# Kernel tuning notes

Hardware: AMD Instinct MI355X
Metric: run time of the kernel (lower is better)

Reference implementation:

```python
import jax, jax.numpy as jnp
import numpy as np

BS, NE, DM, DR = 4, 48, 64, 64

def setup_inputs() -> dict:
    key = jax.random.key(0)
    ks = jax.random.split(key, 8)
    ht = jax.random.normal(ks[0], (BS, NE, NE, DR), dtype=jnp.float32)
    factor = jax.random.normal(ks[1], (BS, NE, NE, NE, DM), dtype=jnp.float32)
    ent_numbers = jax.random.randint(ks[2], (BS,), NE // 2, NE + 1).astype(jnp.int32)
    ent_numbers = ent_numbers.at[0].set(NE)  # max(ent_numbers) must equal ne
    s_c = 1.0 / np.sqrt(DM + DR)
    W_c = jax.random.uniform(ks[3], (DM + DR, DM), jnp.float32, -s_c, s_c)
    b_c = jax.random.uniform(ks[4], (DM,), jnp.float32, -s_c, s_c)
    v_w = jax.random.uniform(ks[5], (DM,), jnp.float32, -1.0 / np.sqrt(DM), 1.0 / np.sqrt(DM))
    s_f = 1.0 / np.sqrt(DM)
    W_fc = jax.random.uniform(ks[6], (DM, DR), jnp.float32, -s_f, s_f)
    b_fc = jax.random.uniform(ks[7], (DR,), jnp.float32, -s_f, s_f)
    ln_g = jnp.ones((DR,), jnp.float32)
    ln_b = jnp.zeros((DR,), jnp.float32)
    return {"ht": ht, "factor": factor, "W_c": W_c, "b_c": b_c, "v_w": v_w,
            "W_fc": W_fc, "b_fc": b_fc, "ln_g": ln_g, "ln_b": ln_b,
            "ent_numbers": ent_numbers}


def reference(ht, factor, W_c, b_c, v_w, W_fc, b_fc, ln_g, ln_b, ent_numbers):
    # factor_type == 'sib'; dropout in eval mode (identity)
    bs, ne, _, dr = ht.shape
    ha = factor                                   # b,i,j,k,dm
    hb = jnp.transpose(factor, (0, 1, 3, 2, 4))   # b,i,k,j,dm -> swap of obj axes
    total_h = jnp.concatenate([ha, hb], axis=3)   # b,i,j,2k,dm
    n2 = total_h.shape[3]
    ht_b = jnp.broadcast_to(ht[:, :, :, None, :], (bs, ne, ne, n2, dr))
    comb = jnp.concatenate([ht_b, total_h], axis=-1)          # b,i,j,2k,dr+dm
    h = jax.nn.gelu(comb @ W_c + b_c, approximate=False)      # exact erf GELU like torch nn.GELU()
    energy = jnp.einsum('bijkd,d->bijk', h, v_w)              # b,i,j,2ne
    # masks: valid[b,e] = e < ent_numbers[b]; mask3d[b,i,j,k] = valid_i & valid_j & valid_k
    idx = jnp.arange(ne)
    valid = idx[None, :] < ent_numbers[:, None]               # b,ne
    mask3d = valid[:, :, None, None] & valid[:, None, :, None] & valid[:, None, None, :]
    eye = jnp.eye(ne, dtype=bool)
    m1 = eye[None, None, :, :] | ~mask3d                      # b,i,j,k  (eye over (j,k))
    attn_mask = jnp.concatenate([m1, m1], axis=-1)            # b,i,j,2ne
    energy = jnp.where(attn_mask, jnp.float32(-10000.0), energy)
    attention = jax.nn.softmax(energy, axis=-1)
    output = jnp.einsum('bijk,bijkd->bijd', attention, total_h)
    output = output @ W_fc + b_fc + ht                        # fc + residual
    mu = jnp.mean(output, axis=-1, keepdims=True)
    var = jnp.mean(jnp.square(output - mu), axis=-1, keepdims=True)
    return ln_g * (output - mu) * jax.lax.rsqrt(var + 1e-6) + ln_b
```

## Files before the change

### kernel.cpp

```cpp
#include <hip/hip_runtime.h>
#include <math.h>
#include <stdint.h>

#define BS 4
#define NE 48
#define DM 64
#define DR 64
#define N2 96

typedef const __attribute__((address_space(1))) uint32_t* gptr_t;
typedef __attribute__((address_space(3))) uint32_t* lptr_t;

__device__ __forceinline__ float wsum(float v) {
#pragma unroll
    for (int m = 1; m < 64; m <<= 1) v += __shfl_xor(v, m, 64);
    return v;
}
__device__ __forceinline__ float wmax(float v) {
#pragma unroll
    for (int m = 1; m < 64; m <<= 1) v = fmaxf(v, __shfl_xor(v, m, 64));
    return v;
}

__device__ __forceinline__ float erf_approx(float x) {
    float ax = fabsf(x);
    float t  = __builtin_amdgcn_rcpf(fmaf(0.3275911f, ax, 1.0f));
    float p  = t * (0.254829592f +
               t * (-0.284496736f +
               t * (1.421413741f +
               t * (-1.453152027f +
               t * 1.061405429f))));
    float e  = __expf(-ax * ax);
    float r  = fmaf(-p, e, 1.0f);
    return copysignf(r, x);
}
__device__ __forceinline__ float gelu_exact(float x) {
    return 0.5f * x * (1.0f + erf_approx(x * 0.70710678118654752440f));
}

__global__ __launch_bounds__(256, 3)
void hgnn_kernel(const float* __restrict__ ht,
                 const float* __restrict__ factor,
                 const float* __restrict__ W_c,
                 const float* __restrict__ b_c,
                 const float* __restrict__ v_w,
                 const float* __restrict__ W_fc,
                 const float* __restrict__ b_fc,
                 const float* __restrict__ ln_g,
                 const float* __restrict__ ln_b,
                 const int* __restrict__ ent_numbers,
                 float* __restrict__ out) {
    __shared__ float sTh[N2][DM];
    __shared__ float sHt[DR];
    __shared__ float sE[N2];
    __shared__ float sA[N2];
    __shared__ float sPart[4][DM];
    __shared__ float sOut[DM];

    const int tid  = threadIdx.x;
    const int lane = tid & 63;
    const int wave = tid >> 6;

    const int orig = blockIdx.x;
    const int bid  = (orig & 7) * (BS * NE * NE / 8) + (orig >> 3);

    const int b   = bid / (NE * NE);
    const int rem = bid - b * NE * NE;
    const int i   = rem / NE;
    const int j   = rem - i * NE;

    const int ent = ent_numbers[b];
    const bool row_valid = (i < ent) && (j < ent);

    {
        const float* fbase = factor + (size_t)((b * NE + i) * NE + j) * NE * DM;
        const float4* srcA = (const float4*)fbase;
#pragma unroll
        for (int n = 0; n < 3; ++n) {
            const int idx0 = n * 256 + wave * 64;
            const float4* g = srcA + idx0 + lane;
            __builtin_amdgcn_global_load_lds(
                (gptr_t)g,
                (lptr_t)((char*)&sTh[0][0] + (size_t)idx0 * 16),
                16, 0, 0);
        }
        const float* fb2 = factor + (size_t)(b * NE + i) * NE * NE * DM + (size_t)j * DM;
#pragma unroll
        for (int n = 0; n < 3; ++n) {
            const int idx0 = n * 256 + wave * 64;
            const int idx  = idx0 + lane;
            const int k    = idx >> 4;
            const int r4   = idx & 15;
            const float4* g = (const float4*)(fb2 + (size_t)k * NE * DM) + r4;
            __builtin_amdgcn_global_load_lds(
                (gptr_t)g,
                (lptr_t)((char*)&sTh[0][0] + (size_t)(NE * 256) + (size_t)idx0 * 16),
                16, 0, 0);
        }
    }

    if (tid < DR) sHt[tid] = ht[((size_t)(b * NE + i) * NE + j) * DR + tid];

    float wcol[64];
#pragma unroll
    for (int r = 0; r < 64; ++r) wcol[r] = W_c[(size_t)(DM + r) * DM + lane];
#pragma unroll
    for (int r = 0; r < 64; ++r) asm volatile("" : "+v"(wcol[r]));

    const float bc = b_c[lane];
    const float vw = v_w[lane];

    __syncthreads();

    float htc = bc;
    {
        const float4* htv = (const float4*)sHt;
#pragma unroll
        for (int r4 = 0; r4 < 16; ++r4) {
            float4 t = htv[r4];
            htc = fmaf(t.x, W_c[(4 * r4 + 0) * DM + lane], htc);
            htc = fmaf(t.y, W_c[(4 * r4 + 1) * DM + lane], htc);
            htc = fmaf(t.z, W_c[(4 * r4 + 2) * DM + lane], htc);
            htc = fmaf(t.w, W_c[(4 * r4 + 3) * DM + lane], htc);
        }
    }

#pragma unroll 1
    for (int t = 0; t < 12; ++t) {
        const int k2a = 8 * t + wave;
        const int k2b = k2a + 4;
        const int ka  = (k2a >= NE) ? (k2a - NE) : k2a;
        const int kb  = (k2b >= NE) ? (k2b - NE) : k2b;
        const bool va = row_valid && (ka != j) && (ka < ent);
        const bool vb = row_valid && (kb != j) && (kb < ent);
        if (!va && !vb) {
            if (lane == 0) { sE[k2a] = -10000.0f; sE[k2b] = -10000.0f; }
            continue;
        }
        float a0 = 0.f, a1 = 0.f, a2 = 0.f, a3 = 0.f;
        float b0 = 0.f, b1 = 0.f, b2 = 0.f, b3 = 0.f;
        const float4* ra = (const float4*)(&sTh[k2a][0]);
        const float4* rb = (const float4*)(&sTh[k2b][0]);
#pragma unroll
        for (int r4 = 0; r4 < 16; ++r4) {
            float4 ta = ra[r4];
            float4 tb = rb[r4];
            a0 = fmaf(ta.x, wcol[4 * r4 + 0], a0);
            b0 = fmaf(tb.x, wcol[4 * r4 + 0], b0);
            a1 = fmaf(ta.y, wcol[4 * r4 + 1], a1);
            b1 = fmaf(tb.y, wcol[4 * r4 + 1], b1);
            a2 = fmaf(ta.z, wcol[4 * r4 + 2], a2);
            b2 = fmaf(tb.z, wcol[4 * r4 + 2], b2);
            a3 = fmaf(ta.w, wcol[4 * r4 + 3], a3);
            b3 = fmaf(tb.w, wcol[4 * r4 + 3], b3);
        }
        float xa = htc + ((a0 + a1) + (a2 + a3));
        float xb = htc + ((b0 + b1) + (b2 + b3));
        float ea = wsum(gelu_exact(xa) * vw);
        float eb = wsum(gelu_exact(xb) * vw);
        if (lane == 0) {
            sE[k2a] = va ? ea : -10000.0f;
            sE[k2b] = vb ? eb : -10000.0f;
        }
    }
    __syncthreads();

    float v0 = sE[lane];
    float v1 = (lane < 32) ? sE[64 + lane] : -3.0e38f;
    float mx = wmax(fmaxf(v0, v1));
    float e0 = expf(v0 - mx);
    float e1 = (lane < 32) ? expf(v1 - mx) : 0.0f;
    float sm = wsum(e0 + e1);
    float inv = 1.0f / sm;
    if (wave == 0) {
        sA[lane] = e0 * inv;
        if (lane < 32) sA[64 + lane] = e1 * inv;
    }
    __syncthreads();

    {
        float acc = 0.0f;
#pragma unroll
        for (int t = 0; t < 24; ++t) {
            const int k2 = 4 * t + wave;
            acc = fmaf(sA[k2], sTh[k2][lane], acc);
        }
        sPart[wave][lane] = acc;
    }
    __syncthreads();
    if (tid < DM)
        sOut[tid] = sPart[0][tid] + sPart[1][tid] + sPart[2][tid] + sPart[3][tid];
    __syncthreads();

    if (wave == 0) {
        float acc = b_fc[lane] + sHt[lane];
        const float4* ov = (const float4*)sOut;
#pragma unroll
        for (int r4 = 0; r4 < 16; ++r4) {
            float4 t4 = ov[r4];
            acc = fmaf(t4.x, W_fc[(4 * r4 + 0) * DM + lane], acc);
            acc = fmaf(t4.y, W_fc[(4 * r4 + 1) * DM + lane], acc);
            acc = fmaf(t4.z, W_fc[(4 * r4 + 2) * DM + lane], acc);
            acc = fmaf(t4.w, W_fc[(4 * r4 + 3) * DM + lane], acc);
        }
        float mu  = wsum(acc) * (1.0f / 64.0f);
        float d   = acc - mu;
        float var = wsum(d * d) * (1.0f / 64.0f);
        float y   = ln_g[lane] * d * rsqrtf(var + 1e-6f) + ln_b[lane];
        out[((size_t)(b * NE + i) * NE + j) * DM + lane] = y;
    }
}

extern "C" void kernel_launch(void* const* d_in, const int* in_sizes, int n_in,
                              void* d_out, int out_size, void* d_ws, size_t ws_size,
                              hipStream_t stream) {
    const float* ht   = (const float*)d_in[0];
    const float* fac  = (const float*)d_in[1];
    const float* W_c  = (const float*)d_in[2];
    const float* b_c  = (const float*)d_in[3];
    const float* v_w  = (const float*)d_in[4];
    const float* W_fc = (const float*)d_in[5];
    const float* b_fc = (const float*)d_in[6];
    const float* ln_g = (const float*)d_in[7];
    const float* ln_b = (const float*)d_in[8];
    const int*   ent  = (const int*)d_in[9];
    float* out = (float*)d_out;

    dim3 grid(BS * NE * NE);
    hgnn_kernel<<<grid, 256, 0, stream>>>(ht, fac, W_c, b_c, v_w, W_fc, b_fc,
                                          ln_g, ln_b, ent, out);
}
```

Baseline: 340.8 us.

## Process four rows per wave iteration, raise occupancy bound, use fast exp in softmax

The energy loop now handles four k-rows per wave per iteration instead of two, with interleaved shuffle reductions for the four sums. Launch bounds go from 3 to 4 blocks per CU and the asm barrier pinning wcol in registers is removed, so the compiler may spill or rematerialize under the tighter budget. The softmax switches expf to __expf. The wider unroll raises ILP and reuses each weight register across more rows, but the stricter register cap risks spills.

```diff
diff --git a/kernel.cpp b/kernel.cpp
--- a/kernel.cpp
+++ b/kernel.cpp
@@ -38,7 +38,7 @@
     return 0.5f * x * (1.0f + erf_approx(x * 0.70710678118654752440f));
 }
 
-__global__ __launch_bounds__(256, 3)
+__global__ __launch_bounds__(256, 4)
 void hgnn_kernel(const float* __restrict__ ht,
                  const float* __restrict__ factor,
                  const float* __restrict__ W_c,
@@ -104,8 +104,6 @@
     float wcol[64];
 #pragma unroll
     for (int r = 0; r < 64; ++r) wcol[r] = W_c[(size_t)(DM + r) * DM + lane];
-#pragma unroll
-    for (int r = 0; r < 64; ++r) asm volatile("" : "+v"(wcol[r]));
 
     const float bc = b_c[lane];
     const float vw = v_w[lane];
@@ -126,41 +124,65 @@
     }
 
 #pragma unroll 1
-    for (int t = 0; t < 12; ++t) {
-        const int k2a = 8 * t + wave;
-        const int k2b = k2a + 4;
-        const int ka  = (k2a >= NE) ? (k2a - NE) : k2a;
-        const int kb  = (k2b >= NE) ? (k2b - NE) : k2b;
-        const bool va = row_valid && (ka != j) && (ka < ent);
-        const bool vb = row_valid && (kb != j) && (kb < ent);
-        if (!va && !vb) {
-            if (lane == 0) { sE[k2a] = -10000.0f; sE[k2b] = -10000.0f; }
+    for (int t = 0; t < 6; ++t) {
+        const int k0 = 16 * t + wave;
+        bool v[4];
+#pragma unroll
+        for (int q = 0; q < 4; ++q) {
+            const int k2 = k0 + 4 * q;
+            const int kk = (k2 >= NE) ? (k2 - NE) : k2;
+            v[q] = row_valid && (kk != j) && (kk < ent);
+        }
+        if (!(v[0] | v[1] | v[2] | v[3])) {
+            if (lane == 0) {
+                sE[k0]      = -10000.0f;
+                sE[k0 + 4]  = -10000.0f;
+                sE[k0 + 8]  = -10000.0f;
+                sE[k0 + 12] = -10000.0f;
+            }
             continue;
         }
-        float a0 = 0.f, a1 = 0.f, a2 = 0.f, a3 = 0.f;
-        float b0 = 0.f, b1 = 0.f, b2 = 0.f, b3 = 0.f;
-        const float4* ra = (const float4*)(&sTh[k2a][0]);
-        const float4* rb = (const float4*)(&sTh[k2b][0]);
+        float ac0 = 0.f, ac1 = 0.f, ac2 = 0.f, ac3 = 0.f;
+        const float4* r0 = (const float4*)(&sTh[k0][0]);
+        const float4* r1 = (const float4*)(&sTh[k0 + 4][0]);
+        const float4* r2 = (const float4*)(&sTh[k0 + 8][0]);
+        const float4* r3 = (const float4*)(&sTh[k0 + 12][0]);
 #pragma unroll
         for (int r4 = 0; r4 < 16; ++r4) {
-            float4 ta = ra[r4];
-            float4 tb = rb[r4];
-            a0 = fmaf(ta.x, wcol[4 * r4 + 0], a0);
-            b0 = fmaf(tb.x, wcol[4 * r4 + 0], b0);
-            a1 = fmaf(ta.y, wcol[4 * r4 + 1], a1);
-            b1 = fmaf(tb.y, wcol[4 * r4 + 1], b1);
-            a2 = fmaf(ta.z, wcol[4 * r4 + 2], a2);
-            b2 = fmaf(tb.z, wcol[4 * r4 + 2], b2);
-            a3 = fmaf(ta.w, wcol[4 * r4 + 3], a3);
-            b3 = fmaf(tb.w, wcol[4 * r4 + 3], b3);
-        }
-        float xa = htc + ((a0 + a1) + (a2 + a3));
-        float xb = htc + ((b0 + b1) + (b2 + b3));
-        float ea = wsum(gelu_exact(xa) * vw);
-        float eb = wsum(gelu_exact(xb) * vw);
+            float4 t0 = r0[r4];
+            float4 t1 = r1[r4];
+            float4 t2 = r2[r4];
+            float4 t3 = r3[r4];
+            float w0 = wcol[4 * r4 + 0];
+            ac0 = fmaf(t0.x, w0, ac0); ac1 = fmaf(t1.x, w0, ac1);
+            ac2 = fmaf(t2.x, w0, ac2); ac3 = fmaf(t3.x, w0, ac3);
+            float w1 = wcol[4 * r4 + 1];
+            ac0 = fmaf(t0.y, w1, ac0); ac1 = fmaf(t1.y, w1, ac1);
+            ac2 = fmaf(t2.y, w1, ac2); ac3 = fmaf(t3.y, w1, ac3);
+            float w2 = wcol[4 * r4 + 2];
+            ac0 = fmaf(t0.z, w2, ac0); ac1 = fmaf(t1.z, w2, ac1);
+            ac2 = fmaf(t2.z, w2, ac2); ac3 = fmaf(t3.z, w2, ac3);
+            float w3 = wcol[4 * r4 + 3];
+            ac0 = fmaf(t0.w, w3, ac0); ac1 = fmaf(t1.w, w3, ac1);
+            ac2 = fmaf(t2.w, w3, ac2); ac3 = fmaf(t3.w, w3, ac3);
+        }
+        float s0 = gelu_exact(htc + ac0) * vw;
+        float s1 = gelu_exact(htc + ac1) * vw;
+        float s2 = gelu_exact(htc + ac2) * vw;
+        float s3 = gelu_exact(htc + ac3) * vw;
+#pragma unroll
+        for (int m = 1; m < 64; m <<= 1) {
+            float u0 = __shfl_xor(s0, m, 64);
+            float u1 = __shfl_xor(s1, m, 64);
+            float u2 = __shfl_xor(s2, m, 64);
+            float u3 = __shfl_xor(s3, m, 64);
+            s0 += u0; s1 += u1; s2 += u2; s3 += u3;
+        }
         if (lane == 0) {
-            sE[k2a] = va ? ea : -10000.0f;
-            sE[k2b] = vb ? eb : -10000.0f;
+            sE[k0]      = v[0] ? s0 : -10000.0f;
+            sE[k0 + 4]  = v[1] ? s1 : -10000.0f;
+            sE[k0 + 8]  = v[2] ? s2 : -10000.0f;
+            sE[k0 + 12] = v[3] ? s3 : -10000.0f;
         }
     }
     __syncthreads();
@@ -168,8 +190,8 @@
     float v0 = sE[lane];
     float v1 = (lane < 32) ? sE[64 + lane] : -3.0e38f;
     float mx = wmax(fmaxf(v0, v1));
-    float e0 = expf(v0 - mx);
-    float e1 = (lane < 32) ? expf(v1 - mx) : 0.0f;
+    float e0 = __expf(v0 - mx);
+    float e1 = (lane < 32) ? __expf(v1 - mx) : 0.0f;
     float sm = wsum(e0 + e1);
     float inv = 1.0f / sm;
     if (wave == 0) {
```

After: 329.4 us. -3.3%, faster.
